# Optimization experiments

Measured on AMD Instinct MI355X. Metric: run time of the kernel, lower is better.

## Reference

```python
import jax, jax.numpy as jnp
import numpy as np

B, T, D = 32, 512, 1024  # batch, timesteps, features == units (residual add requires D == units)


def _layer_norm(x, gamma, beta, eps=1e-3):  # Keras LayerNormalization default eps=1e-3, axis=-1
    m = jnp.mean(x, axis=-1, keepdims=True)
    v = jnp.var(x, axis=-1, keepdims=True)
    return (x - m) * jax.lax.rsqrt(v + eps) * gamma + beta


def setup_inputs() -> dict:
    key = jax.random.key(0)
    ks = jax.random.split(key, 4)
    units = D
    # unit_forget_bias=True: forget-gate bias initialized to ones (gate order i, f, c, o)
    bias = jnp.concatenate([jnp.zeros((units,)), jnp.ones((units,)), jnp.zeros((2 * units,))]).astype(jnp.float32)
    return {
        "x": jax.random.normal(ks[0], (B, T, D), dtype=jnp.float32),
        "ln1_gamma": jnp.ones((D,), jnp.float32),
        "ln1_beta": jnp.zeros((D,), jnp.float32),
        "kernel": jax.random.normal(ks[1], (D, 4 * units), dtype=jnp.float32) * 0.02,
        "recurrent_kernel": jax.random.normal(ks[2], (units, 4 * units), dtype=jnp.float32) * 0.02,
        "bias": bias,
        "ln2_gamma": jnp.ones((D,), jnp.float32),
        "ln2_beta": jnp.zeros((D,), jnp.float32),
    }


def reference(x, ln1_gamma, ln1_beta, kernel, recurrent_kernel, bias, ln2_gamma, ln2_beta):
    xn = _layer_norm(x, ln1_gamma, ln1_beta)
    units = recurrent_kernel.shape[0]

    def step(carry, xt):  # xt: [B, D]
        h, c = carry
        z = xt @ kernel + h @ recurrent_kernel + bias  # [B, 4U]
        i, f, g, o = jnp.split(z, 4, axis=-1)  # Keras gate order i, f, c~, o
        c_new = jax.nn.sigmoid(f) * c + jax.nn.sigmoid(i) * jnp.tanh(g)
        h_new = jax.nn.sigmoid(o) * jnp.tanh(c_new)
        return (h_new, c_new), None

    h0 = jnp.zeros((x.shape[0], units), x.dtype)
    (h_last, _), _ = jax.lax.scan(step, (h0, h0), jnp.swapaxes(xn, 0, 1))  # scan over T
    # Keras RNN (return_sequences=False) yields only the final hidden state [B, U];
    # dropout is identity at inference; Add broadcasts it over the time axis.
    out = _layer_norm(xn + h_last[:, None, :], ln2_gamma, ln2_beta)
    return out
```

## Files before the change

### kernel.cpp

```cpp
#include <hip/hip_runtime.h>

typedef unsigned short u16;
typedef unsigned int   u32;
typedef unsigned long long u64;
typedef __attribute__((ext_vector_type(8)))  short  short8v;
typedef __attribute__((ext_vector_type(4)))  float  f32x4;
typedef __attribute__((ext_vector_type(4)))  unsigned short ushort4v;
typedef __attribute__((ext_vector_type(4)))  u32 u32x4;

#define B_   32
#define T_   512
#define D_   1024
#define N4_  4096
#define NWG  256

#define OFF_XN   0ull
#define OFF_ZX   33554432ull
#define OFF_KT   167772160ull
#define OFF_RT   176160768ull
#define OFF_HB   184549376ull
#define OFF_FLG  184680448ull

__device__ inline u16 f2bf(float f) {
  union { float f; u32 u; } x; x.f = f;
  u32 r = x.u + 0x7FFFu + ((x.u >> 16) & 1u);
  return (u16)(r >> 16);
}
__device__ inline float bf2f(u16 h) {
  union { u32 u; float f; } x; x.u = ((u32)h) << 16; return x.f;
}
__device__ inline float sigm(float x) { return 1.f / (1.f + __expf(-x)); }
__device__ inline float tanh_fast(float x) {
  float e = __expf(2.f * x);
  return 1.f - 2.f / (e + 1.f);
}

__global__ __launch_bounds__(256) void init_kernel(u32* hbuf, u32* flags) {
  int i = blockIdx.x * 256 + threadIdx.x;
  if (i < 32768) hbuf[i] = 0u;
  if (i < NWG)   flags[i * 16] = 0u;
}

__global__ __launch_bounds__(256) void ln1_kernel(const float* __restrict__ x,
    const float* __restrict__ gam, const float* __restrict__ bet, u16* __restrict__ xn) {
  int row = blockIdx.x; int tid = threadIdx.x;
  const float* xr = x + (size_t)row * D_;
  float4 v = *(const float4*)(xr + tid * 4);
  float s  = v.x + v.y + v.z + v.w;
  float ss = v.x*v.x + v.y*v.y + v.z*v.z + v.w*v.w;
  #pragma unroll
  for (int o = 32; o > 0; o >>= 1) { s += __shfl_down(s, o); ss += __shfl_down(ss, o); }
  __shared__ float red[8];
  int w = tid >> 6, l = tid & 63;
  if (l == 0) { red[w] = s; red[4 + w] = ss; }
  __syncthreads();
  s  = red[0] + red[1] + red[2] + red[3];
  ss = red[4] + red[5] + red[6] + red[7];
  float mean = s * (1.f / D_);
  float var  = ss * (1.f / D_) - mean * mean;
  float rstd = rsqrtf(var + 1e-3f);
  float4 g = *(const float4*)(gam + tid * 4);
  float4 b = *(const float4*)(bet + tid * 4);
  ushort4v o4;
  o4.x = f2bf((v.x - mean) * rstd * g.x + b.x);
  o4.y = f2bf((v.y - mean) * rstd * g.y + b.y);
  o4.z = f2bf((v.z - mean) * rstd * g.z + b.z);
  o4.w = f2bf((v.w - mean) * rstd * g.w + b.w);
  *(ushort4v*)(xn + (size_t)row * D_ + tid * 4) = o4;
}

__global__ __launch_bounds__(256) void transpose_bf16(const float* __restrict__ W, u16* __restrict__ WT) {
  __shared__ float tile[32][33];
  int c0 = blockIdx.x * 32, r0 = blockIdx.y * 32;
  int tx = threadIdx.x, ty = threadIdx.y;
  #pragma unroll
  for (int i = ty; i < 32; i += 8)
    tile[i][tx] = W[(size_t)(r0 + i) * N4_ + c0 + tx];
  __syncthreads();
  #pragma unroll
  for (int i = ty; i < 32; i += 8)
    WT[(size_t)(c0 + i) * D_ + r0 + tx] = f2bf(tile[tx][i]);
}

__global__ __launch_bounds__(256) void gemm_xk(const u16* __restrict__ A, const u16* __restrict__ Bt,
    const float* __restrict__ bias, u16* __restrict__ Zx) {
  __shared__ u16 As[128 * 32];
  __shared__ u16 Bs[128 * 32];
  int tid = threadIdx.x;
  int bm = blockIdx.x >> 5, bn = blockIdx.x & 31;
  int w = tid >> 6, l = tid & 63;
  int srow = tid >> 2, sk = (tid & 3) * 8;
  const u16* Ag = A  + (size_t)(bm * 128 + srow) * D_ + sk;
  const u16* Bg = Bt + (size_t)(bn * 128 + srow) * D_ + sk;
  int sb0 = (srow * 64 + sk * 2)          ^ ((srow & 3) << 4);
  int sb1 = ((srow + 64) * 64 + sk * 2)   ^ ((srow & 3) << 4);
  int wm = w >> 1, wn = w & 1;
  int frow = l & 15, fko = (l >> 4) * 16;
  f32x4 acc[4][4];
  #pragma unroll
  for (int mi = 0; mi < 4; ++mi)
    #pragma unroll
    for (int ni = 0; ni < 4; ++ni)
      #pragma unroll
      for (int j = 0; j < 4; ++j) acc[mi][ni][j] = 0.f;

  short8v ap0 = *(const short8v*)(Ag);
  short8v ap1 = *(const short8v*)(Ag + 64 * (size_t)D_);
  short8v bp0 = *(const short8v*)(Bg);
  short8v bp1 = *(const short8v*)(Bg + 64 * (size_t)D_);

  for (int kt = 0; kt < 32; ++kt) {
    __syncthreads();
    *(short8v*)((char*)As + sb0) = ap0;
    *(short8v*)((char*)As + sb1) = ap1;
    *(short8v*)((char*)Bs + sb0) = bp0;
    *(short8v*)((char*)Bs + sb1) = bp1;
    __syncthreads();
    if (kt < 31) {
      ap0 = *(const short8v*)(Ag + (kt + 1) * 32);
      ap1 = *(const short8v*)(Ag + 64 * (size_t)D_ + (kt + 1) * 32);
      bp0 = *(const short8v*)(Bg + (kt + 1) * 32);
      bp1 = *(const short8v*)(Bg + 64 * (size_t)D_ + (kt + 1) * 32);
    }
    short8v af[4], bfr[4];
    #pragma unroll
    for (int mi = 0; mi < 4; ++mi) {
      int r = wm * 64 + mi * 16 + frow;
      af[mi] = *(const short8v*)((char*)As + ((r * 64 + fko) ^ ((r & 3) << 4)));
    }
    #pragma unroll
    for (int ni = 0; ni < 4; ++ni) {
      int r = wn * 64 + ni * 16 + frow;
      bfr[ni] = *(const short8v*)((char*)Bs + ((r * 64 + fko) ^ ((r & 3) << 4)));
    }
    #pragma unroll
    for (int mi = 0; mi < 4; ++mi)
      #pragma unroll
      for (int ni = 0; ni < 4; ++ni)
        acc[mi][ni] = __builtin_amdgcn_mfma_f32_16x16x32_bf16(af[mi], bfr[ni], acc[mi][ni], 0, 0, 0);
  }
  #pragma unroll
  for (int mi = 0; mi < 4; ++mi) {
    #pragma unroll
    for (int ni = 0; ni < 4; ++ni) {
      int col = bn * 128 + wn * 64 + ni * 16 + (l & 15);
      float bv = bias[col];
      int colp = ((col & 1023) << 2) | (col >> 10);
      #pragma unroll
      for (int j = 0; j < 4; ++j) {
        int row = bm * 128 + wm * 64 + mi * 16 + (l >> 4) * 4 + j;
        int zrow = (row & 511) * 32 + (row >> 9);
        Zx[(size_t)zrow * N4_ + colp] = f2bf(acc[mi][ni][j] + bv);
      }
    }
  }
}

__global__ __launch_bounds__(512) __attribute__((amdgpu_waves_per_eu(2, 2)))
void lstm_scan(const u16* __restrict__ Zx,
    const u16* __restrict__ RT, u16* hbuf, float* h_last, u32* flags) {
  __shared__ u16   h_lds[16 * D_];
  __shared__ float z_lds[8 * 16 * 36];
  int tid = threadIdx.x;
  int wg = blockIdx.x;
  int ug = wg >> 1, bh = wg & 1;
  int w = tid >> 6, l = tid & 63;
  int ks = w;
  int fr = l & 15, hi = l >> 4;

  short8v b[4][2];
  #pragma unroll
  for (int ch = 0; ch < 2; ++ch) {
    int c = ch * 16 + fr;
    const u16* Rp = RT + (size_t)((c & 3) * 1024 + ug * 8 + (c >> 2)) * D_
                  + ks * 128 + hi * 8;
    #pragma unroll
    for (int kt = 0; kt < 4; ++kt) b[kt][ch] = *(const short8v*)(Rp + kt * 32);
  }
  #pragma unroll
  for (int kt = 0; kt < 4; ++kt) {
    asm volatile("" : "+v"(b[kt][0]));
    asm volatile("" : "+v"(b[kt][1]));
  }

  int abase = fr * 2048 + ks * 256 + hi * 16;
  int asw = (fr & 7) << 4;
  int grow = tid >> 3, gu = tid & 7;
  const u16* zx_p = Zx + (size_t)(bh * 16 + grow) * N4_ + (ug * 8 + gu) * 4;
  int hoff = (bh * 16 + grow) * D_ + ug * 8 + gu;
  float c = 0.f;
  const u32* fp0 = flags + (size_t)l * 16;
  const u32* fp1 = flags + (size_t)(64 + l) * 16;
  const u32* fp2 = flags + (size_t)(128 + l) * 16;
  const u32* fp3 = flags + (size_t)(192 + l) * 16;

  #pragma unroll 1
  for (int t = 0; t < T_; ++t) {
    u64 zq = 0;
    if (tid < 128) zq = *(const u64*)(zx_p + (size_t)t * B_ * N4_);
    __builtin_amdgcn_sched_barrier(0);

    if (w == 0) {
      while (true) {
        u32 f0 = __hip_atomic_load(fp0, __ATOMIC_RELAXED, __HIP_MEMORY_SCOPE_AGENT);
        u32 f1 = __hip_atomic_load(fp1, __ATOMIC_RELAXED, __HIP_MEMORY_SCOPE_AGENT);
        u32 f2 = __hip_atomic_load(fp2, __ATOMIC_RELAXED, __HIP_MEMORY_SCOPE_AGENT);
        u32 f3 = __hip_atomic_load(fp3, __ATOMIC_RELAXED, __HIP_MEMORY_SCOPE_AGENT);
        u32 t32 = (u32)t;
        if (__all((int)(f0 >= t32 && f1 >= t32 && f2 >= t32 && f3 >= t32))) break;
      }
    }
    __builtin_amdgcn_s_barrier();
    __builtin_amdgcn_sched_barrier(0);

    const char* hbp = (const char*)hbuf + (size_t)(t & 1) * 65536 + (size_t)bh * 32768;
    u32x4 hv[4];
    #pragma unroll
    for (int j = 0; j < 4; ++j) {
      const char* p = hbp + j * 8192 + tid * 16;
      asm volatile("global_load_dwordx4 %0, %1, off sc0 sc1"
                   : "=&v"(hv[j]) : "v"(p) : "memory");
    }
    asm volatile("s_waitcnt vmcnt(0)" ::: "memory");
    __builtin_amdgcn_sched_barrier(0);
    #pragma unroll
    for (int j = 0; j < 4; ++j) {
      int byte = j * 8192 + tid * 16;
      int row = byte >> 11;
      *(u32x4*)((char*)h_lds + (byte ^ ((row & 7) << 4))) = hv[j];
    }
    __syncthreads();

    f32x4 acc0, acc1;
    #pragma unroll
    for (int i = 0; i < 4; ++i) { acc0[i] = 0.f; acc1[i] = 0.f; }
    #pragma unroll
    for (int kt = 0; kt < 4; ++kt) {
      short8v a = *(const short8v*)((const char*)h_lds + ((abase + kt * 64) ^ asw));
      acc0 = __builtin_amdgcn_mfma_f32_16x16x32_bf16(a, b[kt][0], acc0, 0, 0, 0);
      acc1 = __builtin_amdgcn_mfma_f32_16x16x32_bf16(a, b[kt][1], acc1, 0, 0, 0);
    }
    #pragma unroll
    for (int j = 0; j < 4; ++j) {
      int rowD = hi * 4 + j;
      z_lds[(ks * 16 + rowD) * 36 + fr]      = acc0[j];
      z_lds[(ks * 16 + rowD) * 36 + 16 + fr] = acc1[j];
    }
    __syncthreads();

    if (tid < 128) {
      float z0 = bf2f((u16)(zq        & 0xFFFFu));
      float z1 = bf2f((u16)((zq >> 16) & 0xFFFFu));
      float z2 = bf2f((u16)((zq >> 32) & 0xFFFFu));
      float z3 = bf2f((u16)((zq >> 48) & 0xFFFFu));
      #pragma unroll
      for (int kss = 0; kss < 8; ++kss) {
        f32x4 zr = *(const f32x4*)&z_lds[(kss * 16 + grow) * 36 + gu * 4];
        z0 += zr[0]; z1 += zr[1]; z2 += zr[2]; z3 += zr[3];
      }
      float cn = sigm(z1) * c + sigm(z0) * tanh_fast(z2);
      float hn = sigm(z3) * tanh_fast(cn);
      c = cn;

      u32 hw = (u32)f2bf(hn);
      u32 nb = __shfl_down(hw, 1);
      if (!(gu & 1)) {
        u32* dst = (u32*)(hbuf + (size_t)((t + 1) & 1) * (B_ * D_) + hoff);
        __hip_atomic_store(dst, hw | (nb << 16), __ATOMIC_RELAXED, __HIP_MEMORY_SCOPE_AGENT);
      }
      if (t == T_ - 1) h_last[hoff] = hn;
    }
    __syncthreads();
    if (tid == 0)
      __hip_atomic_store(flags + (size_t)wg * 16, (u32)(t + 1),
                         __ATOMIC_RELAXED, __HIP_MEMORY_SCOPE_AGENT);
  }
}

__global__ __launch_bounds__(256) void ln2_kernel(const u16* __restrict__ xn,
    const float* __restrict__ h_last, const float* __restrict__ gam,
    const float* __restrict__ bet, float* __restrict__ out) {
  int row = blockIdx.x; int tid = threadIdx.x;
  int bi = row >> 9;
  ushort4v xv = *(const ushort4v*)(xn + (size_t)row * D_ + tid * 4);
  float4 hv = *(const float4*)(h_last + (size_t)bi * D_ + tid * 4);
  float s0 = bf2f(xv.x) + hv.x;
  float s1 = bf2f(xv.y) + hv.y;
  float s2 = bf2f(xv.z) + hv.z;
  float s3 = bf2f(xv.w) + hv.w;
  float s = s0 + s1 + s2 + s3;
  float ss = s0*s0 + s1*s1 + s2*s2 + s3*s3;
  #pragma unroll
  for (int o = 32; o > 0; o >>= 1) { s += __shfl_down(s, o); ss += __shfl_down(ss, o); }
  __shared__ float red[8];
  int w = tid >> 6, l = tid & 63;
  if (l == 0) { red[w] = s; red[4 + w] = ss; }
  __syncthreads();
  s  = red[0] + red[1] + red[2] + red[3];
  ss = red[4] + red[5] + red[6] + red[7];
  float mean = s * (1.f / D_);
  float var  = ss * (1.f / D_) - mean * mean;
  float rstd = rsqrtf(var + 1e-3f);
  float4 g = *(const float4*)(gam + tid * 4);
  float4 b = *(const float4*)(bet + tid * 4);
  float4 o4;
  o4.x = (s0 - mean) * rstd * g.x + b.x;
  o4.y = (s1 - mean) * rstd * g.y + b.y;
  o4.z = (s2 - mean) * rstd * g.z + b.z;
  o4.w = (s3 - mean) * rstd * g.w + b.w;
  *(float4*)(out + (size_t)row * D_ + tid * 4) = o4;
}

extern "C" void kernel_launch(void* const* d_in, const int* in_sizes, int n_in,
                              void* d_out, int out_size, void* d_ws, size_t ws_size,
                              hipStream_t stream) {
  const float* x    = (const float*)d_in[0];
  const float* g1   = (const float*)d_in[1];
  const float* b1   = (const float*)d_in[2];
  const float* Wk   = (const float*)d_in[3];
  const float* Wr   = (const float*)d_in[4];
  const float* bias = (const float*)d_in[5];
  const float* g2   = (const float*)d_in[6];
  const float* b2   = (const float*)d_in[7];
  char* ws = (char*)d_ws;
  u16* xn    = (u16*)(ws + OFF_XN);
  u16* Zx    = (u16*)(ws + OFF_ZX);
  u16* KT    = (u16*)(ws + OFF_KT);
  u16* RT    = (u16*)(ws + OFF_RT);
  u16* hbuf  = (u16*)(ws + OFF_HB);
  u32* flg   = (u32*)(ws + OFF_FLG);
  float* hl  = (float*)(ws + OFF_KT);
  float* out = (float*)d_out;

  init_kernel<<<128, 256, 0, stream>>>((u32*)hbuf, flg);
  ln1_kernel<<<B_ * T_, 256, 0, stream>>>(x, g1, b1, xn);
  transpose_bf16<<<dim3(128, 32), dim3(32, 8), 0, stream>>>(Wk, KT);
  transpose_bf16<<<dim3(128, 32), dim3(32, 8), 0, stream>>>(Wr, RT);
  gemm_xk<<<4096, 256, 0, stream>>>(xn, KT, bias, Zx);
  lstm_scan<<<NWG, 512, 0, stream>>>(Zx, RT, hbuf, hl, flg);
  ln2_kernel<<<B_ * T_, 256, 0, stream>>>(xn, hl, g2, b2, out);
}
```

Measured before the change: 1.568 ms.

## Load h directly into MFMA operands and use per-wave fine-grained flags

Each wave now reads its recurrent-input fragment of h straight from global memory into registers, which removes the LDS staging and one workgroup barrier per step. The z_lds buffer is double-buffered by step parity so the trailing barrier can be dropped. Each of the two writer waves publishes its own flag, and every wave polls only the 32 flags of the producers it actually depends on, instead of wave 0 polling all 256 workgroups. The cost is more uncoalesced global loads of h per wave and more flag traffic overall, and correctness now depends on the per-wave dependency mapping being right.

```diff
diff --git a/kernel.cpp b/kernel.cpp
--- a/kernel.cpp
+++ b/kernel.cpp
@@ -38,7 +38,7 @@
 __global__ __launch_bounds__(256) void init_kernel(u32* hbuf, u32* flags) {
   int i = blockIdx.x * 256 + threadIdx.x;
   if (i < 32768) hbuf[i] = 0u;
-  if (i < NWG)   flags[i * 16] = 0u;
+  if (i < 512)   flags[i * 16] = 0u;
 }
 
 __global__ __launch_bounds__(256) void ln1_kernel(const float* __restrict__ x,
@@ -159,8 +159,7 @@
 __global__ __launch_bounds__(512) __attribute__((amdgpu_waves_per_eu(2, 2)))
 void lstm_scan(const u16* __restrict__ Zx,
     const u16* __restrict__ RT, u16* hbuf, float* h_last, u32* flags) {
-  __shared__ u16   h_lds[16 * D_];
-  __shared__ float z_lds[8 * 16 * 36];
+  __shared__ float z_lds[2][8 * 16 * 36];
   int tid = threadIdx.x;
   int wg = blockIdx.x;
   int ug = wg >> 1, bh = wg & 1;
@@ -183,16 +182,12 @@
     asm volatile("" : "+v"(b[kt][1]));
   }
 
-  int abase = fr * 2048 + ks * 256 + hi * 16;
-  int asw = (fr & 7) << 4;
+  int aoff = (bh * 16 + fr) * 2048 + ks * 256 + hi * 16;
   int grow = tid >> 3, gu = tid & 7;
   const u16* zx_p = Zx + (size_t)(bh * 16 + grow) * N4_ + (ug * 8 + gu) * 4;
   int hoff = (bh * 16 + grow) * D_ + ug * 8 + gu;
   float c = 0.f;
-  const u32* fp0 = flags + (size_t)l * 16;
-  const u32* fp1 = flags + (size_t)(64 + l) * 16;
-  const u32* fp2 = flags + (size_t)(128 + l) * 16;
-  const u32* fp3 = flags + (size_t)(192 + l) * 16;
+  const u32* fpp = flags + (size_t)((((16 * ks + ((l & 31) >> 1)) * 2 + bh) * 2) + (l & 1)) * 16;
 
   #pragma unroll 1
   for (int t = 0; t < T_; ++t) {
@@ -200,51 +195,42 @@
     if (tid < 128) zq = *(const u64*)(zx_p + (size_t)t * B_ * N4_);
     __builtin_amdgcn_sched_barrier(0);
 
-    if (w == 0) {
+    {
+      u32 t32 = (u32)t;
       while (true) {
-        u32 f0 = __hip_atomic_load(fp0, __ATOMIC_RELAXED, __HIP_MEMORY_SCOPE_AGENT);
-        u32 f1 = __hip_atomic_load(fp1, __ATOMIC_RELAXED, __HIP_MEMORY_SCOPE_AGENT);
-        u32 f2 = __hip_atomic_load(fp2, __ATOMIC_RELAXED, __HIP_MEMORY_SCOPE_AGENT);
-        u32 f3 = __hip_atomic_load(fp3, __ATOMIC_RELAXED, __HIP_MEMORY_SCOPE_AGENT);
-        u32 t32 = (u32)t;
-        if (__all((int)(f0 >= t32 && f1 >= t32 && f2 >= t32 && f3 >= t32))) break;
+        u32 f = (l < 32)
+          ? __hip_atomic_load(fpp, __ATOMIC_RELAXED, __HIP_MEMORY_SCOPE_AGENT)
+          : t32;
+        if (__all((int)(f >= t32))) break;
       }
     }
-    __builtin_amdgcn_s_barrier();
     __builtin_amdgcn_sched_barrier(0);
 
-    const char* hbp = (const char*)hbuf + (size_t)(t & 1) * 65536 + (size_t)bh * 32768;
-    u32x4 hv[4];
-    #pragma unroll
-    for (int j = 0; j < 4; ++j) {
-      const char* p = hbp + j * 8192 + tid * 16;
+    const char* ab = (const char*)hbuf + (size_t)(t & 1) * 65536 + aoff;
+    short8v av[4];
+    #pragma unroll
+    for (int kt = 0; kt < 4; ++kt) {
+      const char* p = ab + kt * 64;
       asm volatile("global_load_dwordx4 %0, %1, off sc0 sc1"
-                   : "=&v"(hv[j]) : "v"(p) : "memory");
+                   : "=&v"(av[kt]) : "v"(p) : "memory");
     }
     asm volatile("s_waitcnt vmcnt(0)" ::: "memory");
     __builtin_amdgcn_sched_barrier(0);
-    #pragma unroll
-    for (int j = 0; j < 4; ++j) {
-      int byte = j * 8192 + tid * 16;
-      int row = byte >> 11;
-      *(u32x4*)((char*)h_lds + (byte ^ ((row & 7) << 4))) = hv[j];
-    }
-    __syncthreads();
 
     f32x4 acc0, acc1;
     #pragma unroll
     for (int i = 0; i < 4; ++i) { acc0[i] = 0.f; acc1[i] = 0.f; }
     #pragma unroll
     for (int kt = 0; kt < 4; ++kt) {
-      short8v a = *(const short8v*)((const char*)h_lds + ((abase + kt * 64) ^ asw));
-      acc0 = __builtin_amdgcn_mfma_f32_16x16x32_bf16(a, b[kt][0], acc0, 0, 0, 0);
-      acc1 = __builtin_amdgcn_mfma_f32_16x16x32_bf16(a, b[kt][1], acc1, 0, 0, 0);
-    }
+      acc0 = __builtin_amdgcn_mfma_f32_16x16x32_bf16(av[kt], b[kt][0], acc0, 0, 0, 0);
+      acc1 = __builtin_amdgcn_mfma_f32_16x16x32_bf16(av[kt], b[kt][1], acc1, 0, 0, 0);
+    }
+    float* zp = z_lds[t & 1];
     #pragma unroll
     for (int j = 0; j < 4; ++j) {
       int rowD = hi * 4 + j;
-      z_lds[(ks * 16 + rowD) * 36 + fr]      = acc0[j];
-      z_lds[(ks * 16 + rowD) * 36 + 16 + fr] = acc1[j];
+      zp[(ks * 16 + rowD) * 36 + fr]      = acc0[j];
+      zp[(ks * 16 + rowD) * 36 + 16 + fr] = acc1[j];
     }
     __syncthreads();
 
@@ -255,7 +241,7 @@
       float z3 = bf2f((u16)((zq >> 48) & 0xFFFFu));
       #pragma unroll
       for (int kss = 0; kss < 8; ++kss) {
-        f32x4 zr = *(const f32x4*)&z_lds[(kss * 16 + grow) * 36 + gu * 4];
+        f32x4 zr = *(const f32x4*)&zp[(kss * 16 + grow) * 36 + gu * 4];
         z0 += zr[0]; z1 += zr[1]; z2 += zr[2]; z3 += zr[3];
       }
       float cn = sigm(z1) * c + sigm(z0) * tanh_fast(z2);
@@ -269,11 +255,11 @@
         __hip_atomic_store(dst, hw | (nb << 16), __ATOMIC_RELAXED, __HIP_MEMORY_SCOPE_AGENT);
       }
       if (t == T_ - 1) h_last[hoff] = hn;
-    }
-    __syncthreads();
-    if (tid == 0)
-      __hip_atomic_store(flags + (size_t)wg * 16, (u32)(t + 1),
-                         __ATOMIC_RELAXED, __HIP_MEMORY_SCOPE_AGENT);
+      asm volatile("s_waitcnt vmcnt(0)" ::: "memory");
+      if (l == 0)
+        __hip_atomic_store(flags + (size_t)(wg * 2 + w) * 16, (u32)(t + 1),
+                           __ATOMIC_RELAXED, __HIP_MEMORY_SCOPE_AGENT);
+    }
   }
 }
 
```

Measured after the change: 1.939 ms. +23.7%, slower.

## Cut per-step barriers in LSTM scan with per-wave h loads and double-buffered z

Applied to the files above, without the earlier changes.

Each wave now loads from global memory only the slice of h it needs and writes it to its own LDS region, so the barrier between the h staging and the MFMA reads is gone. The z partial-sum buffer is double-buffered so the end-of-step barrier can be dropped. Wave 0 alone handles the gate math for two units per lane and publishes the flag after waiting for its h stores to complete. This shortens the serial critical path of each timestep. The cost is redundant global loads of h across waves and correctness that depends on wave 0 doing all the ordering.

```diff
diff --git a/kernel.cpp b/kernel.cpp
--- a/kernel.cpp
+++ b/kernel.cpp
@@ -159,8 +159,8 @@
 __global__ __launch_bounds__(512) __attribute__((amdgpu_waves_per_eu(2, 2)))
 void lstm_scan(const u16* __restrict__ Zx,
     const u16* __restrict__ RT, u16* hbuf, float* h_last, u32* flags) {
-  __shared__ u16   h_lds[16 * D_];
-  __shared__ float z_lds[8 * 16 * 36];
+  __shared__ u16   h_w[8 * 2048];
+  __shared__ float z_lds[2][8 * 16 * 36];
   int tid = threadIdx.x;
   int wg = blockIdx.x;
   int ug = wg >> 1, bh = wg & 1;
@@ -183,12 +183,13 @@
     asm volatile("" : "+v"(b[kt][1]));
   }
 
-  int abase = fr * 2048 + ks * 256 + hi * 16;
-  int asw = (fr & 7) << 4;
-  int grow = tid >> 3, gu = tid & 7;
-  const u16* zx_p = Zx + (size_t)(bh * 16 + grow) * N4_ + (ug * 8 + gu) * 4;
-  int hoff = (bh * 16 + grow) * D_ + ug * 8 + gu;
-  float c = 0.f;
+  int sgbase = (bh * 16 + fr) * 2048 + ks * 256;
+  int slbase = ks * 4096 + fr * 256;
+  int swz = (fr & 15) << 4;
+  int grow = l >> 2, gup = (l & 3) * 2;
+  const u16* zx_p = Zx + (size_t)(bh * 16 + grow) * N4_ + (ug * 8 + gup) * 4;
+  int hoff = (bh * 16 + grow) * D_ + ug * 8 + gup;
+  float c0 = 0.f, c1 = 0.f;
   const u32* fp0 = flags + (size_t)l * 16;
   const u32* fp1 = flags + (size_t)(64 + l) * 16;
   const u32* fp2 = flags + (size_t)(128 + l) * 16;
@@ -196,84 +197,88 @@
 
   #pragma unroll 1
   for (int t = 0; t < T_; ++t) {
-    u64 zq = 0;
-    if (tid < 128) zq = *(const u64*)(zx_p + (size_t)t * B_ * N4_);
-    __builtin_amdgcn_sched_barrier(0);
-
+    u32x4 zq;
     if (w == 0) {
+      zq = *(const u32x4*)(zx_p + (size_t)t * B_ * N4_);
+      __builtin_amdgcn_sched_barrier(0);
+      u32 t32 = (u32)t;
       while (true) {
         u32 f0 = __hip_atomic_load(fp0, __ATOMIC_RELAXED, __HIP_MEMORY_SCOPE_AGENT);
         u32 f1 = __hip_atomic_load(fp1, __ATOMIC_RELAXED, __HIP_MEMORY_SCOPE_AGENT);
         u32 f2 = __hip_atomic_load(fp2, __ATOMIC_RELAXED, __HIP_MEMORY_SCOPE_AGENT);
         u32 f3 = __hip_atomic_load(fp3, __ATOMIC_RELAXED, __HIP_MEMORY_SCOPE_AGENT);
-        u32 t32 = (u32)t;
         if (__all((int)(f0 >= t32 && f1 >= t32 && f2 >= t32 && f3 >= t32))) break;
       }
     }
     __builtin_amdgcn_s_barrier();
     __builtin_amdgcn_sched_barrier(0);
 
-    const char* hbp = (const char*)hbuf + (size_t)(t & 1) * 65536 + (size_t)bh * 32768;
-    u32x4 hv[4];
-    #pragma unroll
-    for (int j = 0; j < 4; ++j) {
-      const char* p = hbp + j * 8192 + tid * 16;
-      asm volatile("global_load_dwordx4 %0, %1, off sc0 sc1"
-                   : "=&v"(hv[j]) : "v"(p) : "memory");
-    }
-    asm volatile("s_waitcnt vmcnt(0)" ::: "memory");
-    __builtin_amdgcn_sched_barrier(0);
-    #pragma unroll
-    for (int j = 0; j < 4; ++j) {
-      int byte = j * 8192 + tid * 16;
-      int row = byte >> 11;
-      *(u32x4*)((char*)h_lds + (byte ^ ((row & 7) << 4))) = hv[j];
-    }
-    __syncthreads();
-
+    {
+      const char* gb = (const char*)hbuf + (size_t)(t & 1) * 65536 + sgbase;
+      u32x4 hv[4];
+      #pragma unroll
+      for (int j = 0; j < 4; ++j) {
+        const char* p = gb + hi * 16 + j * 64;
+        asm volatile("global_load_dwordx4 %0, %1, off sc0 sc1"
+                     : "=&v"(hv[j]) : "v"(p) : "memory");
+      }
+      asm volatile("s_waitcnt vmcnt(0)" ::: "memory");
+      __builtin_amdgcn_sched_barrier(0);
+      #pragma unroll
+      for (int j = 0; j < 4; ++j) {
+        int cofs = hi * 16 + j * 64;
+        *(u32x4*)((char*)h_w + slbase + (cofs ^ swz)) = hv[j];
+      }
+    }
     f32x4 acc0, acc1;
     #pragma unroll
     for (int i = 0; i < 4; ++i) { acc0[i] = 0.f; acc1[i] = 0.f; }
     #pragma unroll
     for (int kt = 0; kt < 4; ++kt) {
-      short8v a = *(const short8v*)((const char*)h_lds + ((abase + kt * 64) ^ asw));
+      short8v a = *(const short8v*)((const char*)h_w + slbase + ((hi * 16 + kt * 64) ^ swz));
       acc0 = __builtin_amdgcn_mfma_f32_16x16x32_bf16(a, b[kt][0], acc0, 0, 0, 0);
       acc1 = __builtin_amdgcn_mfma_f32_16x16x32_bf16(a, b[kt][1], acc1, 0, 0, 0);
     }
+    float* zp = z_lds[t & 1];
     #pragma unroll
     for (int j = 0; j < 4; ++j) {
       int rowD = hi * 4 + j;
-      z_lds[(ks * 16 + rowD) * 36 + fr]      = acc0[j];
-      z_lds[(ks * 16 + rowD) * 36 + 16 + fr] = acc1[j];
+      zp[(ks * 16 + rowD) * 36 + fr]      = acc0[j];
+      zp[(ks * 16 + rowD) * 36 + 16 + fr] = acc1[j];
     }
     __syncthreads();
 
-    if (tid < 128) {
-      float z0 = bf2f((u16)(zq        & 0xFFFFu));
-      float z1 = bf2f((u16)((zq >> 16) & 0xFFFFu));
-      float z2 = bf2f((u16)((zq >> 32) & 0xFFFFu));
-      float z3 = bf2f((u16)((zq >> 48) & 0xFFFFu));
+    if (w == 0) {
+      float z0a = bf2f((u16)(zq[0] & 0xFFFFu)), z1a = bf2f((u16)(zq[0] >> 16));
+      float z2a = bf2f((u16)(zq[1] & 0xFFFFu)), z3a = bf2f((u16)(zq[1] >> 16));
+      float z0b = bf2f((u16)(zq[2] & 0xFFFFu)), z1b = bf2f((u16)(zq[2] >> 16));
+      float z2b = bf2f((u16)(zq[3] & 0xFFFFu)), z3b = bf2f((u16)(zq[3] >> 16));
       #pragma unroll
       for (int kss = 0; kss < 8; ++kss) {
-        f32x4 zr = *(const f32x4*)&z_lds[(kss * 16 + grow) * 36 + gu * 4];
-        z0 += zr[0]; z1 += zr[1]; z2 += zr[2]; z3 += zr[3];
-      }
-      float cn = sigm(z1) * c + sigm(z0) * tanh_fast(z2);
-      float hn = sigm(z3) * tanh_fast(cn);
-      c = cn;
-
-      u32 hw = (u32)f2bf(hn);
-      u32 nb = __shfl_down(hw, 1);
-      if (!(gu & 1)) {
-        u32* dst = (u32*)(hbuf + (size_t)((t + 1) & 1) * (B_ * D_) + hoff);
-        __hip_atomic_store(dst, hw | (nb << 16), __ATOMIC_RELAXED, __HIP_MEMORY_SCOPE_AGENT);
-      }
-      if (t == T_ - 1) h_last[hoff] = hn;
-    }
-    __syncthreads();
-    if (tid == 0)
-      __hip_atomic_store(flags + (size_t)wg * 16, (u32)(t + 1),
-                         __ATOMIC_RELAXED, __HIP_MEMORY_SCOPE_AGENT);
+        const float* zr = &zp[(kss * 16 + grow) * 36 + gup * 4];
+        f32x4 za = *(const f32x4*)(zr);
+        f32x4 zb = *(const f32x4*)(zr + 4);
+        z0a += za[0]; z1a += za[1]; z2a += za[2]; z3a += za[3];
+        z0b += zb[0]; z1b += zb[1]; z2b += zb[2]; z3b += zb[3];
+      }
+      float cn0 = sigm(z1a) * c0 + sigm(z0a) * tanh_fast(z2a);
+      float hn0 = sigm(z3a) * tanh_fast(cn0);
+      float cn1 = sigm(z1b) * c1 + sigm(z0b) * tanh_fast(z2b);
+      float hn1 = sigm(z3b) * tanh_fast(cn1);
+      c0 = cn0; c1 = cn1;
+
+      u32 word = (u32)f2bf(hn0) | ((u32)f2bf(hn1) << 16);
+      u32* dst = (u32*)(hbuf + (size_t)((t + 1) & 1) * (B_ * D_) + hoff);
+      __hip_atomic_store(dst, word, __ATOMIC_RELAXED, __HIP_MEMORY_SCOPE_AGENT);
+      if (t == T_ - 1) {
+        h_last[hoff]     = hn0;
+        h_last[hoff + 1] = hn1;
+      }
+      asm volatile("s_waitcnt vmcnt(0)" ::: "memory");
+      if (l == 0)
+        __hip_atomic_store(flags + (size_t)wg * 16, (u32)(t + 1),
+                           __ATOMIC_RELAXED, __HIP_MEMORY_SCOPE_AGENT);
+    }
   }
 }
 
```

New measurement: 2.199 ms. 40.2% more time.

## Fuse input projection GEMM into recurrent scan and halve flag polling

Applied to the files above, without the earlier changes.

Removes the separate x·K GEMM and its Zx buffer. Each scan workgroup keeps its slice of the input kernel in registers and computes the input-projection MFMAs for step t before waiting on the inter-workgroup flags, so that work can hide behind the synchronisation wait. The bias is added in fp32 from registers, and each workgroup now polls only the flags of workgroups sharing its batch half. This trades the Zx write and read traffic and one launch for extra per-step xn loads and doubled B-fragment register pressure inside the latency-critical scan.

```diff
diff --git a/kernel.cpp b/kernel.cpp
--- a/kernel.cpp
+++ b/kernel.cpp
@@ -15,7 +15,7 @@
 #define NWG  256
 
 #define OFF_XN   0ull
-#define OFF_ZX   33554432ull
+#define OFF_HL   33554432ull
 #define OFF_KT   167772160ull
 #define OFF_RT   176160768ull
 #define OFF_HB   184549376ull
@@ -82,83 +82,10 @@
     WT[(size_t)(c0 + i) * D_ + r0 + tx] = f2bf(tile[tx][i]);
 }
 
-__global__ __launch_bounds__(256) void gemm_xk(const u16* __restrict__ A, const u16* __restrict__ Bt,
-    const float* __restrict__ bias, u16* __restrict__ Zx) {
-  __shared__ u16 As[128 * 32];
-  __shared__ u16 Bs[128 * 32];
-  int tid = threadIdx.x;
-  int bm = blockIdx.x >> 5, bn = blockIdx.x & 31;
-  int w = tid >> 6, l = tid & 63;
-  int srow = tid >> 2, sk = (tid & 3) * 8;
-  const u16* Ag = A  + (size_t)(bm * 128 + srow) * D_ + sk;
-  const u16* Bg = Bt + (size_t)(bn * 128 + srow) * D_ + sk;
-  int sb0 = (srow * 64 + sk * 2)          ^ ((srow & 3) << 4);
-  int sb1 = ((srow + 64) * 64 + sk * 2)   ^ ((srow & 3) << 4);
-  int wm = w >> 1, wn = w & 1;
-  int frow = l & 15, fko = (l >> 4) * 16;
-  f32x4 acc[4][4];
-  #pragma unroll
-  for (int mi = 0; mi < 4; ++mi)
-    #pragma unroll
-    for (int ni = 0; ni < 4; ++ni)
-      #pragma unroll
-      for (int j = 0; j < 4; ++j) acc[mi][ni][j] = 0.f;
-
-  short8v ap0 = *(const short8v*)(Ag);
-  short8v ap1 = *(const short8v*)(Ag + 64 * (size_t)D_);
-  short8v bp0 = *(const short8v*)(Bg);
-  short8v bp1 = *(const short8v*)(Bg + 64 * (size_t)D_);
-
-  for (int kt = 0; kt < 32; ++kt) {
-    __syncthreads();
-    *(short8v*)((char*)As + sb0) = ap0;
-    *(short8v*)((char*)As + sb1) = ap1;
-    *(short8v*)((char*)Bs + sb0) = bp0;
-    *(short8v*)((char*)Bs + sb1) = bp1;
-    __syncthreads();
-    if (kt < 31) {
-      ap0 = *(const short8v*)(Ag + (kt + 1) * 32);
-      ap1 = *(const short8v*)(Ag + 64 * (size_t)D_ + (kt + 1) * 32);
-      bp0 = *(const short8v*)(Bg + (kt + 1) * 32);
-      bp1 = *(const short8v*)(Bg + 64 * (size_t)D_ + (kt + 1) * 32);
-    }
-    short8v af[4], bfr[4];
-    #pragma unroll
-    for (int mi = 0; mi < 4; ++mi) {
-      int r = wm * 64 + mi * 16 + frow;
-      af[mi] = *(const short8v*)((char*)As + ((r * 64 + fko) ^ ((r & 3) << 4)));
-    }
-    #pragma unroll
-    for (int ni = 0; ni < 4; ++ni) {
-      int r = wn * 64 + ni * 16 + frow;
-      bfr[ni] = *(const short8v*)((char*)Bs + ((r * 64 + fko) ^ ((r & 3) << 4)));
-    }
-    #pragma unroll
-    for (int mi = 0; mi < 4; ++mi)
-      #pragma unroll
-      for (int ni = 0; ni < 4; ++ni)
-        acc[mi][ni] = __builtin_amdgcn_mfma_f32_16x16x32_bf16(af[mi], bfr[ni], acc[mi][ni], 0, 0, 0);
-  }
-  #pragma unroll
-  for (int mi = 0; mi < 4; ++mi) {
-    #pragma unroll
-    for (int ni = 0; ni < 4; ++ni) {
-      int col = bn * 128 + wn * 64 + ni * 16 + (l & 15);
-      float bv = bias[col];
-      int colp = ((col & 1023) << 2) | (col >> 10);
-      #pragma unroll
-      for (int j = 0; j < 4; ++j) {
-        int row = bm * 128 + wm * 64 + mi * 16 + (l >> 4) * 4 + j;
-        int zrow = (row & 511) * 32 + (row >> 9);
-        Zx[(size_t)zrow * N4_ + colp] = f2bf(acc[mi][ni][j] + bv);
-      }
-    }
-  }
-}
-
 __global__ __launch_bounds__(512) __attribute__((amdgpu_waves_per_eu(2, 2)))
-void lstm_scan(const u16* __restrict__ Zx,
-    const u16* __restrict__ RT, u16* hbuf, float* h_last, u32* flags) {
+void lstm_scan(const u16* __restrict__ xn, const u16* __restrict__ KT,
+    const u16* __restrict__ RT, const float* __restrict__ bias,
+    u16* hbuf, float* h_last, u32* flags) {
   __shared__ u16   h_lds[16 * D_];
   __shared__ float z_lds[8 * 16 * 36];
   int tid = threadIdx.x;
@@ -168,46 +95,65 @@
   int ks = w;
   int fr = l & 15, hi = l >> 4;
 
-  short8v b[4][2];
+  short8v bR[4][2], bK[4][2];
   #pragma unroll
   for (int ch = 0; ch < 2; ++ch) {
     int c = ch * 16 + fr;
-    const u16* Rp = RT + (size_t)((c & 3) * 1024 + ug * 8 + (c >> 2)) * D_
+    size_t rowoff = (size_t)((c & 3) * 1024 + ug * 8 + (c >> 2)) * D_
                   + ks * 128 + hi * 8;
-    #pragma unroll
-    for (int kt = 0; kt < 4; ++kt) b[kt][ch] = *(const short8v*)(Rp + kt * 32);
+    const u16* Rp = RT + rowoff;
+    const u16* Kp = KT + rowoff;
+    #pragma unroll
+    for (int kt = 0; kt < 4; ++kt) {
+      bR[kt][ch] = *(const short8v*)(Rp + kt * 32);
+      bK[kt][ch] = *(const short8v*)(Kp + kt * 32);
+    }
   }
   #pragma unroll
   for (int kt = 0; kt < 4; ++kt) {
-    asm volatile("" : "+v"(b[kt][0]));
-    asm volatile("" : "+v"(b[kt][1]));
-  }
-
+    asm volatile("" : "+v"(bR[kt][0]));
+    asm volatile("" : "+v"(bR[kt][1]));
+    asm volatile("" : "+v"(bK[kt][0]));
+    asm volatile("" : "+v"(bK[kt][1]));
+  }
+
+  const u16* xnp = xn + (size_t)(bh * 16 + fr) * 512 * D_ + ks * 128 + hi * 8;
   int abase = fr * 2048 + ks * 256 + hi * 16;
   int asw = (fr & 7) << 4;
   int grow = tid >> 3, gu = tid & 7;
-  const u16* zx_p = Zx + (size_t)(bh * 16 + grow) * N4_ + (ug * 8 + gu) * 4;
   int hoff = (bh * 16 + grow) * D_ + ug * 8 + gu;
   float c = 0.f;
-  const u32* fp0 = flags + (size_t)l * 16;
-  const u32* fp1 = flags + (size_t)(64 + l) * 16;
-  const u32* fp2 = flags + (size_t)(128 + l) * 16;
-  const u32* fp3 = flags + (size_t)(192 + l) * 16;
+  float bi0 = 0.f, bf0 = 0.f, bg0 = 0.f, bo0 = 0.f;
+  if (tid < 128) {
+    int u = ug * 8 + gu;
+    bi0 = bias[u]; bf0 = bias[1024 + u]; bg0 = bias[2048 + u]; bo0 = bias[3072 + u];
+  }
+  const u32* fp0 = flags + (size_t)(2 * l + bh) * 16;
+  const u32* fp1 = flags + (size_t)(2 * (64 + l) + bh) * 16;
 
   #pragma unroll 1
   for (int t = 0; t < T_; ++t) {
-    u64 zq = 0;
-    if (tid < 128) zq = *(const u64*)(zx_p + (size_t)t * B_ * N4_);
+    f32x4 acc0, acc1;
+    #pragma unroll
+    for (int i = 0; i < 4; ++i) { acc0[i] = 0.f; acc1[i] = 0.f; }
+    {
+      short8v ax[4];
+      #pragma unroll
+      for (int kt = 0; kt < 4; ++kt) ax[kt] = *(const short8v*)(xnp + kt * 32);
+      #pragma unroll
+      for (int kt = 0; kt < 4; ++kt) {
+        acc0 = __builtin_amdgcn_mfma_f32_16x16x32_bf16(ax[kt], bK[kt][0], acc0, 0, 0, 0);
+        acc1 = __builtin_amdgcn_mfma_f32_16x16x32_bf16(ax[kt], bK[kt][1], acc1, 0, 0, 0);
+      }
+    }
     __builtin_amdgcn_sched_barrier(0);
 
     if (w == 0) {
+      u32 t32 = (u32)t;
       while (true) {
         u32 f0 = __hip_atomic_load(fp0, __ATOMIC_RELAXED, __HIP_MEMORY_SCOPE_AGENT);
         u32 f1 = __hip_atomic_load(fp1, __ATOMIC_RELAXED, __HIP_MEMORY_SCOPE_AGENT);
-        u32 f2 = __hip_atomic_load(fp2, __ATOMIC_RELAXED, __HIP_MEMORY_SCOPE_AGENT);
-        u32 f3 = __hip_atomic_load(fp3, __ATOMIC_RELAXED, __HIP_MEMORY_SCOPE_AGENT);
-        u32 t32 = (u32)t;
-        if (__all((int)(f0 >= t32 && f1 >= t32 && f2 >= t32 && f3 >= t32))) break;
+        if (__all((int)(f0 >= t32 && f1 >= t32))) break;
       }
     }
     __builtin_amdgcn_s_barrier();
@@ -231,14 +177,11 @@
     }
     __syncthreads();
 
-    f32x4 acc0, acc1;
-    #pragma unroll
-    for (int i = 0; i < 4; ++i) { acc0[i] = 0.f; acc1[i] = 0.f; }
     #pragma unroll
     for (int kt = 0; kt < 4; ++kt) {
       short8v a = *(const short8v*)((const char*)h_lds + ((abase + kt * 64) ^ asw));
-      acc0 = __builtin_amdgcn_mfma_f32_16x16x32_bf16(a, b[kt][0], acc0, 0, 0, 0);
-      acc1 = __builtin_amdgcn_mfma_f32_16x16x32_bf16(a, b[kt][1], acc1, 0, 0, 0);
+      acc0 = __builtin_amdgcn_mfma_f32_16x16x32_bf16(a, bR[kt][0], acc0, 0, 0, 0);
+      acc1 = __builtin_amdgcn_mfma_f32_16x16x32_bf16(a, bR[kt][1], acc1, 0, 0, 0);
     }
     #pragma unroll
     for (int j = 0; j < 4; ++j) {
@@ -249,10 +192,7 @@
     __syncthreads();
 
     if (tid < 128) {
-      float z0 = bf2f((u16)(zq        & 0xFFFFu));
-      float z1 = bf2f((u16)((zq >> 16) & 0xFFFFu));
-      float z2 = bf2f((u16)((zq >> 32) & 0xFFFFu));
-      float z3 = bf2f((u16)((zq >> 48) & 0xFFFFu));
+      float z0 = bi0, z1 = bf0, z2 = bg0, z3 = bo0;
       #pragma unroll
       for (int kss = 0; kss < 8; ++kss) {
         f32x4 zr = *(const f32x4*)&z_lds[(kss * 16 + grow) * 36 + gu * 4];
@@ -274,6 +214,7 @@
     if (tid == 0)
       __hip_atomic_store(flags + (size_t)wg * 16, (u32)(t + 1),
                          __ATOMIC_RELAXED, __HIP_MEMORY_SCOPE_AGENT);
+    xnp += D_;
   }
 }
 
@@ -324,19 +265,17 @@
   const float* b2   = (const float*)d_in[7];
   char* ws = (char*)d_ws;
   u16* xn    = (u16*)(ws + OFF_XN);
-  u16* Zx    = (u16*)(ws + OFF_ZX);
   u16* KT    = (u16*)(ws + OFF_KT);
   u16* RT    = (u16*)(ws + OFF_RT);
   u16* hbuf  = (u16*)(ws + OFF_HB);
   u32* flg   = (u32*)(ws + OFF_FLG);
-  float* hl  = (float*)(ws + OFF_KT);
+  float* hl  = (float*)(ws + OFF_HL);
   float* out = (float*)d_out;
 
   init_kernel<<<128, 256, 0, stream>>>((u32*)hbuf, flg);
   ln1_kernel<<<B_ * T_, 256, 0, stream>>>(x, g1, b1, xn);
   transpose_bf16<<<dim3(128, 32), dim3(32, 8), 0, stream>>>(Wk, KT);
   transpose_bf16<<<dim3(128, 32), dim3(32, 8), 0, stream>>>(Wr, RT);
-  gemm_xk<<<4096, 256, 0, stream>>>(xn, KT, bias, Zx);
-  lstm_scan<<<NWG, 512, 0, stream>>>(Zx, RT, hbuf, hl, flg);
+  lstm_scan<<<NWG, 512, 0, stream>>>(xn, KT, RT, bias, hbuf, hl, flg);
   ln2_kernel<<<B_ * T_, 256, 0, stream>>>(xn, hl, g2, b2, out);
 }
```

New measurement: 1.518 ms. -3.2%, faster.
